# Optimization experiments

Hardware: AMD Instinct MI355X
Metric: run time of the kernel (lower is better)

The kernel has to match this reference:

```python
import jax, jax.numpy as jnp
import numpy as np

T, D, N = 131072, 512, 8


def setup_inputs() -> dict:
    key = jax.random.key(0)
    k1, k2, k3, k4 = jax.random.split(key, 4)
    x = jax.random.normal(k1, (T, D), dtype=jnp.float32)
    branch_idx = jax.random.randint(k2, (T,), 0, N, dtype=jnp.int32)
    # module inits weight to identity and bias to zero; use random values
    # (scaled like a trained projection) for a meaningful correctness test
    weight = jax.random.normal(k3, (N, D, D), dtype=jnp.float32) * (1.0 / np.sqrt(D))
    bias = jax.random.normal(k4, (N, D), dtype=jnp.float32) * 0.02
    return {"x": x, "branch_idx": branch_idx, "weight": weight, "bias": bias}


def reference(x, branch_idx, weight, bias):
    # Math: out[t] = x[t] @ weight[branch_idx[t]] + bias[branch_idx[t]]
    # Instead of materializing the gathered (T, D, D) weight tensor (as the
    # naive torch code does), run one dense GEMM per branch and select the
    # rows belonging to that branch. Same result, far less HBM traffic.
    num_branches = weight.shape[0]
    out = jnp.take(bias, branch_idx, axis=0)  # (T, D) gathered bias
    for n in range(num_branches):  # small fixed loop over branches
        mask = (branch_idx == n)[:, None]  # (T, 1)
        out = out + jnp.where(mask, x @ weight[n], jnp.zeros((), x.dtype))
    return out
```

## Files before the change

### kernel.cpp

```cpp
#include <hip/hip_runtime.h>
#include <hip/hip_bf16.h>
#include <stdint.h>

#define T_TOK 131072
#define DIM   512
#define NBR   8
#define BM    64
#define BK    32
#define NKT   (DIM / BK)
#define GT    512
#define MT    288

typedef __attribute__((ext_vector_type(8))) __bf16 bf16x8;
typedef __attribute__((ext_vector_type(4))) float  f32x4;
typedef unsigned short ushort_t;

__device__ __forceinline__ unsigned short f2bf(float f) {
  union { float f; unsigned int u; } v; v.f = f;
  unsigned int r = v.u + 0x7fffu + ((v.u >> 16) & 1u);
  return (unsigned short)(r >> 16);
}


__global__ void k_init(int* counts) {
  if (threadIdx.x < NBR) counts[threadIdx.x] = 0;
}

__global__ __launch_bounds__(512) void k_bhist(const int* __restrict__ bidx,
                                               int* __restrict__ counts) {
  __shared__ int h[NBR];
  if (threadIdx.x < NBR) h[threadIdx.x] = 0;
  __syncthreads();
  int t = blockIdx.x * 512 + threadIdx.x;
  atomicAdd(&h[bidx[t]], 1);
  __syncthreads();
  if (threadIdx.x < NBR) atomicAdd(&counts[threadIdx.x], h[threadIdx.x]);
}

__global__ void k_off(const int* __restrict__ counts, int* __restrict__ offsets,
                      int* __restrict__ cursors) {
  if (threadIdx.x == 0) {
    int s = 0;
    for (int n = 0; n < NBR; ++n) { offsets[n] = s; cursors[n] = s; s += counts[n]; }
  }
}

__global__ __launch_bounds__(512) void k_scatter(const int* __restrict__ bidx,
                                                 int* __restrict__ cursors,
                                                 int* __restrict__ perm) {
  __shared__ int h[NBR], base[NBR];
  if (threadIdx.x < NBR) h[threadIdx.x] = 0;
  __syncthreads();
  int t = blockIdx.x * 512 + threadIdx.x;
  int b = bidx[t];
  int rank = atomicAdd(&h[b], 1);
  __syncthreads();
  if (threadIdx.x < NBR)
    base[threadIdx.x] = atomicAdd(&cursors[threadIdx.x], h[threadIdx.x]);
  __syncthreads();
  perm[base[b] + rank] = t;
}

__global__ __launch_bounds__(256) void k_wtrans(const float* __restrict__ W,
                                                ushort_t* __restrict__ Wt) {
  __shared__ float tile[BK][129];
  int blk = blockIdx.x;
  int b  = blk >> 6;
  int kt = (blk >> 2) & 15;
  int cb = blk & 3;
  int t = threadIdx.x;
  #pragma unroll
  for (int i = 0; i < 4; ++i) {
    int idx4 = i * 256 + t;
    int kr = idx4 >> 5;
    int c4 = idx4 & 31;
    const float* src = W + (((size_t)b * DIM + (size_t)(kt * BK + kr)) * DIM + cb * 128 + c4 * 4);
    float4 v = *(const float4*)src;
    tile[kr][c4 * 4 + 0] = v.x;
    tile[kr][c4 * 4 + 1] = v.y;
    tile[kr][c4 * 4 + 2] = v.z;
    tile[kr][c4 * 4 + 3] = v.w;
  }
  __syncthreads();
  int c  = t >> 1;
  int kh = t & 1;
  unsigned int p[8];
  #pragma unroll
  for (int i = 0; i < 8; ++i) {
    unsigned short lo = f2bf(tile[kh * 16 + i * 2 + 0][c]);
    unsigned short hi = f2bf(tile[kh * 16 + i * 2 + 1][c]);
    p[i] = (unsigned int)lo | ((unsigned int)hi << 16);
  }
  size_t obase = (((size_t)b * 16 + kt) * DIM + (size_t)(cb * 128 + c)) * BK + kh * 16;
  uint4 q0; q0.x = p[0]; q0.y = p[1]; q0.z = p[2]; q0.w = p[3];
  uint4 q1; q1.x = p[4]; q1.y = p[5]; q1.z = p[6]; q1.w = p[7];
  *(uint4*)&Wt[obase]     = q0;
  *(uint4*)&Wt[obase + 8] = q1;
}

__global__ __launch_bounds__(GT, 4)
void k_gemm(const float* __restrict__ x, const float* __restrict__ bias,
            const ushort_t* __restrict__ Wt,
            const int* __restrict__ counts, const int* __restrict__ offsets,
            const int* __restrict__ perm, float* __restrict__ out) {
  __shared__ __align__(16) ushort_t As[NKT * 4 * 64 * 8];
  __shared__ int rowIdx[BM];

  const int tid = threadIdx.x;
  const int l = tid & 63;
  const int w = tid >> 6;

  const int b  = blockIdx.x / MT;
  const int lt = blockIdx.x % MT;
  const int cnt = counts[b];
  const int row0 = lt * BM;
  if (row0 >= cnt) return;
  const int gstart = offsets[b];
  const int vrows = min(BM, cnt - row0);

  if (tid < BM) {
    int r = row0 + tid; if (r >= cnt) r = cnt - 1;
    rowIdx[tid] = perm[gstart + r];
  }
  __syncthreads();

  const int arow = tid >> 3;
  const int kq = tid & 7;
  const float* aptr = x + (size_t)rowIdx[arow] * DIM + kq * 4;
  const int wbase = (((arow >> 4) * 64) + (kq >> 1) * 16 + (arow & 15)) * 8 + (kq & 1) * 4;

  {
    float4 xa = *(const float4*)aptr;
    float4 xb = *(const float4*)(aptr + BK);
    #pragma unroll
    for (int i = 0; i < NKT; ++i) {
      float4 xn;
      if (i + 2 < NKT) xn = *(const float4*)(aptr + (i + 2) * BK);
      ushort4 a4;
      a4.x = f2bf(xa.x); a4.y = f2bf(xa.y); a4.z = f2bf(xa.z); a4.w = f2bf(xa.w);
      *(ushort4*)&As[i * 2048 + wbase] = a4;
      xa = xb; xb = xn;
    }
  }
  __syncthreads();

  const ushort_t* wtile = Wt + (size_t)b * (NKT * BK * DIM);
  int bBase[4];
  #pragma unroll
  for (int cf = 0; cf < 4; ++cf)
    bBase[cf] = (w * 64 + cf * 16 + (l & 15)) * BK + (l >> 4) * 8;

  f32x4 acc[4][4];
  #pragma unroll
  for (int rf = 0; rf < 4; ++rf)
    #pragma unroll
    for (int cf = 0; cf < 4; ++cf) acc[rf][cf] = (f32x4){0.f, 0.f, 0.f, 0.f};

  bf16x8 bq[4];
  #pragma unroll
  for (int cf = 0; cf < 4; ++cf) bq[cf] = *(const bf16x8*)(wtile + bBase[cf]);

  #pragma unroll
  for (int kt = 0; kt < NKT; ++kt) {
    bf16x8 bqn[4];
    if (kt + 1 < NKT) {
      const ushort_t* wtk = wtile + (kt + 1) * (BK * DIM);
      #pragma unroll
      for (int cf = 0; cf < 4; ++cf) bqn[cf] = *(const bf16x8*)(wtk + bBase[cf]);
    }
    bf16x8 af[4];
    #pragma unroll
    for (int rf = 0; rf < 4; ++rf)
      af[rf] = *(const bf16x8*)&As[(kt * 4 + rf) * 512 + l * 8];
    #pragma unroll
    for (int cf = 0; cf < 4; ++cf)
      #pragma unroll
      for (int rf = 0; rf < 4; ++rf)
        acc[rf][cf] = __builtin_amdgcn_mfma_f32_16x16x32_bf16(af[rf], bq[cf], acc[rf][cf], 0, 0, 0);
    if (kt + 1 < NKT) {
      #pragma unroll
      for (int cf = 0; cf < 4; ++cf) bq[cf] = bqn[cf];
    }
  }

  float bv[4];
  #pragma unroll
  for (int cf = 0; cf < 4; ++cf) bv[cf] = bias[b * DIM + w * 64 + cf * 16 + (l & 15)];
  const int rb = (l >> 4) * 4;
  #pragma unroll
  for (int rf = 0; rf < 4; ++rf) {
    #pragma unroll
    for (int j = 0; j < 4; ++j) {
      int r = rf * 16 + rb + j;
      if (r < vrows) {
        float* op = out + (size_t)rowIdx[r] * DIM + w * 64 + (l & 15);
        #pragma unroll
        for (int cf = 0; cf < 4; ++cf) op[cf * 16] = acc[rf][cf][j] + bv[cf];
      }
    }
  }
}

extern "C" void kernel_launch(void* const* d_in, const int* in_sizes, int n_in,
                              void* d_out, int out_size, void* d_ws, size_t ws_size,
                              hipStream_t stream) {
  const float* x    = (const float*)d_in[0];
  const int*   bidx = (const int*)d_in[1];
  const float* W    = (const float*)d_in[2];
  const float* bias = (const float*)d_in[3];
  float* out = (float*)d_out;

  char* ws = (char*)d_ws;
  int* counts  = (int*)(ws + 0);
  int* cursors = (int*)(ws + 64);
  int* offsets = (int*)(ws + 128);
  int* perm    = (int*)(ws + 256);
  ushort_t* Wt = (ushort_t*)(ws + (1u << 20));

  k_init<<<1, 64, 0, stream>>>(counts);
  k_bhist<<<T_TOK / 512, 512, 0, stream>>>(bidx, counts);
  k_off<<<1, 64, 0, stream>>>(counts, offsets, cursors);
  k_scatter<<<T_TOK / 512, 512, 0, stream>>>(bidx, cursors, perm);
  k_wtrans<<<512, 256, 0, stream>>>(W, Wt);
  k_gemm<<<NBR * MT, GT, 0, stream>>>(x, bias, Wt, counts, offsets, perm, out);
}
```

Baseline: 205.8 us.

## Coalesce gathered x loads and stage output through swizzled LDS for float4 stores

```diff
diff --git a/kernel.cpp b/kernel.cpp
--- a/kernel.cpp
+++ b/kernel.cpp
@@ -105,6 +105,7 @@
             const int* __restrict__ perm, float* __restrict__ out) {
   __shared__ __align__(16) ushort_t As[NKT * 4 * 64 * 8];
   __shared__ int rowIdx[BM];
+  float* Ot = (float*)As;
 
   const int tid = threadIdx.x;
   const int l = tid & 63;
@@ -124,22 +125,31 @@
   }
   __syncthreads();
 
-  const int arow = tid >> 3;
-  const int kq = tid & 7;
-  const float* aptr = x + (size_t)rowIdx[arow] * DIM + kq * 4;
-  const int wbase = (((arow >> 4) * 64) + (kq >> 1) * 16 + (arow & 15)) * 8 + (kq & 1) * 4;
-
   {
-    float4 xa = *(const float4*)aptr;
-    float4 xb = *(const float4*)(aptr + BK);
-    #pragma unroll
-    for (int i = 0; i < NKT; ++i) {
-      float4 xn;
-      if (i + 2 < NKT) xn = *(const float4*)(aptr + (i + 2) * BK);
-      ushort4 a4;
-      a4.x = f2bf(xa.x); a4.y = f2bf(xa.y); a4.z = f2bf(xa.z); a4.w = f2bf(xa.w);
-      *(ushort4*)&As[i * 2048 + wbase] = a4;
-      xa = xb; xb = xn;
+    float4 v[8][2];
+    #pragma unroll
+    for (int j = 0; j < 8; ++j) {
+      const float* rp = x + (size_t)rowIdx[w * 8 + j] * DIM;
+      #pragma unroll
+      for (int i = 0; i < 2; ++i)
+        v[j][i] = *(const float4*)(rp + i * 256 + l * 4);
+    }
+    const int rf  = w >> 1;
+    const int Llo = (w & 1) * 8;
+    const int Lhi = (l & 7) >> 1;
+    const int e0  = (l & 1) * 4;
+    const int ktl = l >> 3;
+    #pragma unroll
+    for (int j = 0; j < 8; ++j) {
+      #pragma unroll
+      for (int i = 0; i < 2; ++i) {
+        int f = (i * 8 + ktl) * 4 + rf;
+        int slot = (Lhi * 16 + Llo + j) ^ ktl;
+        ushort4 a4;
+        a4.x = f2bf(v[j][i].x); a4.y = f2bf(v[j][i].y);
+        a4.z = f2bf(v[j][i].z); a4.w = f2bf(v[j][i].w);
+        *(ushort4*)&As[f * 512 + slot * 8 + e0] = a4;
+      }
     }
   }
   __syncthreads();
@@ -168,10 +178,11 @@
       #pragma unroll
       for (int cf = 0; cf < 4; ++cf) bqn[cf] = *(const bf16x8*)(wtk + bBase[cf]);
     }
+    const int lsw = (l ^ (kt & 7)) * 8;
     bf16x8 af[4];
     #pragma unroll
     for (int rf = 0; rf < 4; ++rf)
-      af[rf] = *(const bf16x8*)&As[(kt * 4 + rf) * 512 + l * 8];
+      af[rf] = *(const bf16x8*)&As[(kt * 4 + rf) * 512 + lsw];
     #pragma unroll
     for (int cf = 0; cf < 4; ++cf)
       #pragma unroll
@@ -186,18 +197,40 @@
   float bv[4];
   #pragma unroll
   for (int cf = 0; cf < 4; ++cf) bv[cf] = bias[b * DIM + w * 64 + cf * 16 + (l & 15)];
-  const int rb = (l >> 4) * 4;
-  #pragma unroll
-  for (int rf = 0; rf < 4; ++rf) {
-    #pragma unroll
-    for (int j = 0; j < 4; ++j) {
-      int r = rf * 16 + rb + j;
-      if (r < vrows) {
-        float* op = out + (size_t)rowIdx[r] * DIM + w * 64 + (l & 15);
+
+  __syncthreads();
+  #pragma unroll
+  for (int p = 0; p < 2; ++p) {
+    #pragma unroll
+    for (int rr = 0; rr < 2; ++rr) {
+      int rf = p * 2 + rr;
+      #pragma unroll
+      for (int j = 0; j < 4; ++j) {
+        int rip = rr * 16 + (l >> 4) * 4 + j;
+        int sxk = (rip & 7) << 2;
         #pragma unroll
-        for (int cf = 0; cf < 4; ++cf) op[cf * 16] = acc[rf][cf][j] + bv[cf];
+        for (int cf = 0; cf < 4; ++cf) {
+          int col = w * 64 + cf * 16 + (l & 15);
+          Ot[rip * 512 + (col ^ sxk)] = acc[rf][cf][j] + bv[cf];
+        }
       }
     }
+    __syncthreads();
+    #pragma unroll
+    for (int q = 0; q < 4; ++q) {
+      int rip = w * 4 + q;
+      int grow = p * 32 + rip;
+      if (grow < vrows) {
+        float* op = out + (size_t)rowIdx[grow] * DIM;
+        int s = rip & 7;
+        #pragma unroll
+        for (int h = 0; h < 2; ++h) {
+          float4 vv = *(const float4*)&Ot[rip * 512 + h * 256 + l * 4];
+          *(float4*)(op + h * 256 + ((l ^ s) * 4)) = vv;
+        }
+      }
+    }
+    if (p == 0) __syncthreads();
   }
 }
 
```

Result: slower. 220.9 us (+7.3%).

## Make grouped GEMM persistent with prefetched double-buffered A tiles

Applied to the files above, without the earlier changes.

```diff
diff --git a/kernel.cpp b/kernel.cpp
--- a/kernel.cpp
+++ b/kernel.cpp
@@ -5,11 +5,13 @@
 #define T_TOK 131072
 #define DIM   512
 #define NBR   8
-#define BM    64
+#define BM    32
 #define BK    32
 #define NKT   (DIM / BK)
 #define GT    512
-#define MT    288
+#define MTS   544
+#define NTILE (NBR * MTS)
+#define GRID  1024
 
 typedef __attribute__((ext_vector_type(8))) __bf16 bf16x8;
 typedef __attribute__((ext_vector_type(4))) float  f32x4;
@@ -103,101 +105,147 @@
             const ushort_t* __restrict__ Wt,
             const int* __restrict__ counts, const int* __restrict__ offsets,
             const int* __restrict__ perm, float* __restrict__ out) {
-  __shared__ __align__(16) ushort_t As[NKT * 4 * 64 * 8];
-  __shared__ int rowIdx[BM];
+  __shared__ __align__(16) ushort_t As[2][NKT * 2 * 512];
 
   const int tid = threadIdx.x;
   const int l = tid & 63;
   const int w = tid >> 6;
 
-  const int b  = blockIdx.x / MT;
-  const int lt = blockIdx.x % MT;
-  const int cnt = counts[b];
-  const int row0 = lt * BM;
-  if (row0 >= cnt) return;
-  const int gstart = offsets[b];
-  const int vrows = min(BM, cnt - row0);
-
-  if (tid < BM) {
-    int r = row0 + tid; if (r >= cnt) r = cnt - 1;
-    rowIdx[tid] = perm[gstart + r];
-  }
-  __syncthreads();
-
-  const int arow = tid >> 3;
-  const int kq = tid & 7;
-  const float* aptr = x + (size_t)rowIdx[arow] * DIM + kq * 4;
-  const int wbase = (((arow >> 4) * 64) + (kq >> 1) * 16 + (arow & 15)) * 8 + (kq & 1) * 4;
-
+  int cur_t = blockIdx.x;
+  for (;;) {
+    if (cur_t >= NTILE) return;
+    int b = cur_t / MTS, lt = cur_t - b * MTS;
+    if (lt * BM < counts[b]) break;
+    cur_t += GRID;
+  }
+
+  float4 v[4][2];
   {
-    float4 xa = *(const float4*)aptr;
-    float4 xb = *(const float4*)(aptr + BK);
-    #pragma unroll
-    for (int i = 0; i < NKT; ++i) {
-      float4 xn;
-      if (i + 2 < NKT) xn = *(const float4*)(aptr + (i + 2) * BK);
-      ushort4 a4;
-      a4.x = f2bf(xa.x); a4.y = f2bf(xa.y); a4.z = f2bf(xa.z); a4.w = f2bf(xa.w);
-      *(ushort4*)&As[i * 2048 + wbase] = a4;
-      xa = xb; xb = xn;
-    }
-  }
-  __syncthreads();
-
-  const ushort_t* wtile = Wt + (size_t)b * (NKT * BK * DIM);
-  int bBase[4];
-  #pragma unroll
-  for (int cf = 0; cf < 4; ++cf)
-    bBase[cf] = (w * 64 + cf * 16 + (l & 15)) * BK + (l >> 4) * 8;
-
-  f32x4 acc[4][4];
-  #pragma unroll
-  for (int rf = 0; rf < 4; ++rf)
-    #pragma unroll
-    for (int cf = 0; cf < 4; ++cf) acc[rf][cf] = (f32x4){0.f, 0.f, 0.f, 0.f};
-
-  bf16x8 bq[4];
-  #pragma unroll
-  for (int cf = 0; cf < 4; ++cf) bq[cf] = *(const bf16x8*)(wtile + bBase[cf]);
-
-  #pragma unroll
-  for (int kt = 0; kt < NKT; ++kt) {
-    bf16x8 bqn[4];
-    if (kt + 1 < NKT) {
-      const ushort_t* wtk = wtile + (kt + 1) * (BK * DIM);
-      #pragma unroll
-      for (int cf = 0; cf < 4; ++cf) bqn[cf] = *(const bf16x8*)(wtk + bBase[cf]);
-    }
-    bf16x8 af[4];
-    #pragma unroll
-    for (int rf = 0; rf < 4; ++rf)
-      af[rf] = *(const bf16x8*)&As[(kt * 4 + rf) * 512 + l * 8];
+    int b = cur_t / MTS, lt = cur_t - b * MTS;
+    int cnt = counts[b], g0 = offsets[b];
+    #pragma unroll
+    for (int j = 0; j < 4; ++j) {
+      int r = lt * BM + w * 4 + j;
+      int rr = perm[g0 + (r < cnt ? r : cnt - 1)];
+      const float* rp = x + (size_t)rr * DIM;
+      v[j][0] = *(const float4*)(rp + l * 4);
+      v[j][1] = *(const float4*)(rp + 256 + l * 4);
+    }
+  }
+
+  int cur = 0;
+  for (;;) {
+    int next_t = cur_t + GRID;
+    for (;;) {
+      if (next_t >= NTILE) break;
+      int b = next_t / MTS, lt = next_t - b * MTS;
+      if (lt * BM < counts[b]) break;
+      next_t += GRID;
+    }
+
+    {
+      const int q  = (l & 7) >> 1;
+      const int e0 = (l & 1) * 4;
+      const int h  = l >> 3;
+      const int rf = w >> 2;
+      #pragma unroll
+      for (int j = 0; j < 4; ++j) {
+        const int rlow = (w * 4 + j) & 15;
+        #pragma unroll
+        for (int i = 0; i < 2; ++i) {
+          int kt = i * 8 + h;
+          int Ls = (q * 16 + rlow) ^ h;
+          ushort4 a4;
+          a4.x = f2bf(v[j][i].x); a4.y = f2bf(v[j][i].y);
+          a4.z = f2bf(v[j][i].z); a4.w = f2bf(v[j][i].w);
+          *(ushort4*)&As[cur][(kt * 2 + rf) * 512 + Ls * 8 + e0] = a4;
+        }
+      }
+    }
+    __syncthreads();
+
+    if (next_t < NTILE) {
+      int b = next_t / MTS, lt = next_t - b * MTS;
+      int cnt = counts[b], g0 = offsets[b];
+      #pragma unroll
+      for (int j = 0; j < 4; ++j) {
+        int r = lt * BM + w * 4 + j;
+        int rr = perm[g0 + (r < cnt ? r : cnt - 1)];
+        const float* rp = x + (size_t)rr * DIM;
+        v[j][0] = *(const float4*)(rp + l * 4);
+        v[j][1] = *(const float4*)(rp + 256 + l * 4);
+      }
+    }
+
+    const int bcur = cur_t / MTS;
+    const ushort_t* wtile = Wt + (size_t)bcur * (NKT * BK * DIM);
+    int bBase[4];
     #pragma unroll
     for (int cf = 0; cf < 4; ++cf)
-      #pragma unroll
-      for (int rf = 0; rf < 4; ++rf)
-        acc[rf][cf] = __builtin_amdgcn_mfma_f32_16x16x32_bf16(af[rf], bq[cf], acc[rf][cf], 0, 0, 0);
-    if (kt + 1 < NKT) {
-      #pragma unroll
-      for (int cf = 0; cf < 4; ++cf) bq[cf] = bqn[cf];
-    }
-  }
-
-  float bv[4];
-  #pragma unroll
-  for (int cf = 0; cf < 4; ++cf) bv[cf] = bias[b * DIM + w * 64 + cf * 16 + (l & 15)];
-  const int rb = (l >> 4) * 4;
-  #pragma unroll
-  for (int rf = 0; rf < 4; ++rf) {
-    #pragma unroll
-    for (int j = 0; j < 4; ++j) {
-      int r = rf * 16 + rb + j;
-      if (r < vrows) {
-        float* op = out + (size_t)rowIdx[r] * DIM + w * 64 + (l & 15);
-        #pragma unroll
-        for (int cf = 0; cf < 4; ++cf) op[cf * 16] = acc[rf][cf][j] + bv[cf];
-      }
-    }
+      bBase[cf] = (w * 64 + cf * 16 + (l & 15)) * BK + (l >> 4) * 8;
+
+    f32x4 acc[2][4];
+    #pragma unroll
+    for (int rf = 0; rf < 2; ++rf)
+      #pragma unroll
+      for (int cf = 0; cf < 4; ++cf) acc[rf][cf] = (f32x4){0.f, 0.f, 0.f, 0.f};
+
+    bf16x8 bq[4];
+    #pragma unroll
+    for (int cf = 0; cf < 4; ++cf) bq[cf] = *(const bf16x8*)(wtile + bBase[cf]);
+
+    const ushort_t* asrc = &As[cur][0];
+    #pragma unroll
+    for (int kt = 0; kt < NKT; ++kt) {
+      bf16x8 bqn[4];
+      if (kt + 1 < NKT) {
+        const ushort_t* wtk = wtile + (kt + 1) * (BK * DIM);
+        #pragma unroll
+        for (int cf = 0; cf < 4; ++cf) bqn[cf] = *(const bf16x8*)(wtk + bBase[cf]);
+      }
+      const int lsw = (l ^ (kt & 7)) * 8;
+      bf16x8 af[2];
+      #pragma unroll
+      for (int rf = 0; rf < 2; ++rf)
+        af[rf] = *(const bf16x8*)&asrc[(kt * 2 + rf) * 512 + lsw];
+      #pragma unroll
+      for (int cf = 0; cf < 4; ++cf)
+        #pragma unroll
+        for (int rf = 0; rf < 2; ++rf)
+          acc[rf][cf] = __builtin_amdgcn_mfma_f32_16x16x32_bf16(af[rf], bq[cf], acc[rf][cf], 0, 0, 0);
+      if (kt + 1 < NKT) {
+        #pragma unroll
+        for (int cf = 0; cf < 4; ++cf) bq[cf] = bqn[cf];
+      }
+    }
+
+    {
+      const int ltc = cur_t - bcur * MTS;
+      const int cnt = counts[bcur];
+      const int vrows = min(BM, cnt - ltc * BM);
+      const int g0 = offsets[bcur] + ltc * BM;
+      float bv[4];
+      #pragma unroll
+      for (int cf = 0; cf < 4; ++cf)
+        bv[cf] = bias[bcur * DIM + w * 64 + cf * 16 + (l & 15)];
+      #pragma unroll
+      for (int rf = 0; rf < 2; ++rf) {
+        #pragma unroll
+        for (int j = 0; j < 4; ++j) {
+          int r = rf * 16 + (l >> 4) * 4 + j;
+          if (r < vrows) {
+            int orow = perm[g0 + r];
+            float* op = out + (size_t)orow * DIM + w * 64 + (l & 15);
+            #pragma unroll
+            for (int cf = 0; cf < 4; ++cf) op[cf * 16] = acc[rf][cf][j] + bv[cf];
+          }
+        }
+      }
+    }
+
+    if (next_t >= NTILE) return;
+    cur_t = next_t;
+    cur ^= 1;
   }
 }
 
@@ -222,5 +270,5 @@
   k_off<<<1, 64, 0, stream>>>(counts, offsets, cursors);
   k_scatter<<<T_TOK / 512, 512, 0, stream>>>(bidx, cursors, perm);
   k_wtrans<<<512, 256, 0, stream>>>(W, Wt);
-  k_gemm<<<NBR * MT, GT, 0, stream>>>(x, bias, Wt, counts, offsets, perm, out);
-}
+  k_gemm<<<GRID, GT, 0, stream>>>(x, bias, Wt, counts, offsets, perm, out);
+}
```

New measurement: 266.7 us. +29.6%, slower.

## Replace global branch sort with per-window local sort and pre-converted bf16 x

Applied to the files above, without the earlier changes.

```diff
diff --git a/kernel.cpp b/kernel.cpp
--- a/kernel.cpp
+++ b/kernel.cpp
@@ -5,11 +5,12 @@
 #define T_TOK 131072
 #define DIM   512
 #define NBR   8
-#define BM    64
+#define WIN   512
+#define NWIN  (T_TOK / WIN)
+#define SLCAP 640
+#define NSL   40
 #define BK    32
 #define NKT   (DIM / BK)
-#define GT    512
-#define MT    288
 
 typedef __attribute__((ext_vector_type(8))) __bf16 bf16x8;
 typedef __attribute__((ext_vector_type(4))) float  f32x4;
@@ -19,46 +20,6 @@
   union { float f; unsigned int u; } v; v.f = f;
   unsigned int r = v.u + 0x7fffu + ((v.u >> 16) & 1u);
   return (unsigned short)(r >> 16);
-}
-
-
-__global__ void k_init(int* counts) {
-  if (threadIdx.x < NBR) counts[threadIdx.x] = 0;
-}
-
-__global__ __launch_bounds__(512) void k_bhist(const int* __restrict__ bidx,
-                                               int* __restrict__ counts) {
-  __shared__ int h[NBR];
-  if (threadIdx.x < NBR) h[threadIdx.x] = 0;
-  __syncthreads();
-  int t = blockIdx.x * 512 + threadIdx.x;
-  atomicAdd(&h[bidx[t]], 1);
-  __syncthreads();
-  if (threadIdx.x < NBR) atomicAdd(&counts[threadIdx.x], h[threadIdx.x]);
-}
-
-__global__ void k_off(const int* __restrict__ counts, int* __restrict__ offsets,
-                      int* __restrict__ cursors) {
-  if (threadIdx.x == 0) {
-    int s = 0;
-    for (int n = 0; n < NBR; ++n) { offsets[n] = s; cursors[n] = s; s += counts[n]; }
-  }
-}
-
-__global__ __launch_bounds__(512) void k_scatter(const int* __restrict__ bidx,
-                                                 int* __restrict__ cursors,
-                                                 int* __restrict__ perm) {
-  __shared__ int h[NBR], base[NBR];
-  if (threadIdx.x < NBR) h[threadIdx.x] = 0;
-  __syncthreads();
-  int t = blockIdx.x * 512 + threadIdx.x;
-  int b = bidx[t];
-  int rank = atomicAdd(&h[b], 1);
-  __syncthreads();
-  if (threadIdx.x < NBR)
-    base[threadIdx.x] = atomicAdd(&cursors[threadIdx.x], h[threadIdx.x]);
-  __syncthreads();
-  perm[base[b] + rank] = t;
 }
 
 __global__ __launch_bounds__(256) void k_wtrans(const float* __restrict__ W,
@@ -98,104 +59,160 @@
   *(uint4*)&Wt[obase + 8] = q1;
 }
 
-__global__ __launch_bounds__(GT, 4)
-void k_gemm(const float* __restrict__ x, const float* __restrict__ bias,
-            const ushort_t* __restrict__ Wt,
-            const int* __restrict__ counts, const int* __restrict__ offsets,
-            const int* __restrict__ perm, float* __restrict__ out) {
-  __shared__ __align__(16) ushort_t As[NKT * 4 * 64 * 8];
-  __shared__ int rowIdx[BM];
-
-  const int tid = threadIdx.x;
-  const int l = tid & 63;
-  const int w = tid >> 6;
-
-  const int b  = blockIdx.x / MT;
-  const int lt = blockIdx.x % MT;
-  const int cnt = counts[b];
-  const int row0 = lt * BM;
-  if (row0 >= cnt) return;
-  const int gstart = offsets[b];
-  const int vrows = min(BM, cnt - row0);
-
-  if (tid < BM) {
-    int r = row0 + tid; if (r >= cnt) r = cnt - 1;
-    rowIdx[tid] = perm[gstart + r];
-  }
-  __syncthreads();
-
-  const int arow = tid >> 3;
-  const int kq = tid & 7;
-  const float* aptr = x + (size_t)rowIdx[arow] * DIM + kq * 4;
-  const int wbase = (((arow >> 4) * 64) + (kq >> 1) * 16 + (arow & 15)) * 8 + (kq & 1) * 4;
-
-  {
-    float4 xa = *(const float4*)aptr;
-    float4 xb = *(const float4*)(aptr + BK);
-    #pragma unroll
-    for (int i = 0; i < NKT; ++i) {
-      float4 xn;
-      if (i + 2 < NKT) xn = *(const float4*)(aptr + (i + 2) * BK);
-      ushort4 a4;
-      a4.x = f2bf(xa.x); a4.y = f2bf(xa.y); a4.z = f2bf(xa.z); a4.w = f2bf(xa.w);
-      *(ushort4*)&As[i * 2048 + wbase] = a4;
-      xa = xb; xb = xn;
-    }
-  }
-  __syncthreads();
-
-  const ushort_t* wtile = Wt + (size_t)b * (NKT * BK * DIM);
-  int bBase[4];
+__global__ __launch_bounds__(WIN) void k_sort(const int* __restrict__ bidx,
+                                              unsigned short* __restrict__ smap,
+                                              int* __restrict__ sliceBr,
+                                              int* __restrict__ tsArr) {
+  __shared__ int cnt[NBR], ps[NBR], rankL[WIN], bidL[WIN];
+  const int w = blockIdx.x;
+  const int t = threadIdx.x;
+  if (t < NBR) cnt[t] = 0;
+  __syncthreads();
+  int b = bidx[w * WIN + t];
+  bidL[t] = b;
+  rankL[t] = atomicAdd(&cnt[b], 1);
+  __syncthreads();
+  if (t == 0) {
+    int s = 0;
+    for (int g = 0; g < NBR; ++g) { ps[g] = s; s += (cnt[g] + 15) >> 4; }
+    tsArr[w] = s;
+  }
+  __syncthreads();
+  if (t < NSL) {
+    int br = -1;
+    #pragma unroll
+    for (int g = 0; g < NBR; ++g) {
+      int sc = (cnt[g] + 15) >> 4;
+      if (t >= ps[g] && t < ps[g] + sc) br = g;
+    }
+    sliceBr[w * NSL + t] = br;
+  }
+  smap[w * WIN + t] = (unsigned short)(ps[bidL[t]] * 16 + rankL[t]);
+}
+
+__global__ __launch_bounds__(512) void k_xcvt(const float* __restrict__ x,
+                                              const unsigned short* __restrict__ smap,
+                                              ushort_t* __restrict__ xT, int w0) {
+  __shared__ unsigned short slotL[WIN];
+  const int bid = blockIdx.x;
+  const int w = w0 + (bid >> 2);
+  const int part = bid & 3;
+  const int t = threadIdx.x;
+  slotL[t] = smap[w * WIN + t];
+  __syncthreads();
+  const float4* xp = (const float4*)(x + (size_t)w * (WIN * DIM));
+  ushort_t* xTw = xT + (size_t)(w - w0) * (NKT * SLCAP * BK);
+  #pragma unroll 4
+  for (int i = 0; i < 32; ++i) {
+    int fidx = part * 16384 + i * 512 + t;
+    float4 v = xp[fidx];
+    int row = fidx >> 7;
+    int kq4 = fidx & 127;
+    int kt = kq4 >> 3;
+    int kk = (kq4 & 7) * 4;
+    int slot = slotL[row];
+    ushort4 a4;
+    a4.x = f2bf(v.x); a4.y = f2bf(v.y); a4.z = f2bf(v.z); a4.w = f2bf(v.w);
+    *(ushort4*)&xTw[((size_t)kt * SLCAP + slot) * BK + kk] = a4;
+  }
+}
+
+__global__ __launch_bounds__(1024, 4)
+void k_gemm(const ushort_t* __restrict__ xT, const ushort_t* __restrict__ Wt,
+            const float* __restrict__ bias,
+            const unsigned short* __restrict__ smap,
+            const int* __restrict__ sliceBr, const int* __restrict__ tsArr,
+            float* __restrict__ out, int w0, int WCcur) {
+  __shared__ float OtL[128 * 130];
+  __shared__ int sbrL[NSL];
+
+  const int bid = blockIdx.x;
+  const int wloc = bid % WCcur;
+  const int cb = bid / WCcur;
+  const int w = w0 + wloc;
+  const int t = threadIdx.x;
+  const int l = t & 63;
+  const int wv = t >> 6;
+  const int ts = tsArr[w];
+
+  if (t < NSL) sbrL[t] = sliceBr[w * NSL + t];
+  const unsigned short myslot = smap[w * WIN + (t & 511)];
+  __syncthreads();
+
+  const int sg = wv >> 1;
+  const int ch = wv & 1;
+  const int colbase = cb * 128 + ch * 64;
+
+  const ushort_t* xTw = xT + (size_t)wloc * (NKT * SLCAP * BK);
+  const int aoff = (l & 15) * BK + (l >> 4) * 8;
+  int boff[4];
   #pragma unroll
   for (int cf = 0; cf < 4; ++cf)
-    bBase[cf] = (w * 64 + cf * 16 + (l & 15)) * BK + (l >> 4) * 8;
-
-  f32x4 acc[4][4];
-  #pragma unroll
-  for (int rf = 0; rf < 4; ++rf)
-    #pragma unroll
-    for (int cf = 0; cf < 4; ++cf) acc[rf][cf] = (f32x4){0.f, 0.f, 0.f, 0.f};
-
-  bf16x8 bq[4];
-  #pragma unroll
-  for (int cf = 0; cf < 4; ++cf) bq[cf] = *(const bf16x8*)(wtile + bBase[cf]);
-
-  #pragma unroll
+    boff[cf] = (colbase + cf * 16 + (l & 15)) * BK + (l >> 4) * 8;
+
+  f32x4 acc[5][4];
+  #pragma unroll
+  for (int s = 0; s < 5; ++s)
+    #pragma unroll
+    for (int cf = 0; cf < 4; ++cf) acc[s][cf] = (f32x4){0.f, 0.f, 0.f, 0.f};
+
   for (int kt = 0; kt < NKT; ++kt) {
-    bf16x8 bqn[4];
-    if (kt + 1 < NKT) {
-      const ushort_t* wtk = wtile + (kt + 1) * (BK * DIM);
+    const ushort_t* aplane = xTw + (size_t)kt * (SLCAP * BK);
+    int curbr = -1;
+    bf16x8 bq[4];
+    #pragma unroll
+    for (int s = 0; s < 5; ++s) {
+      const int gs = sg * 5 + s;
+      if (gs < ts) {
+        int br = sbrL[gs];
+        if (br != curbr) {
+          curbr = br;
+          const ushort_t* wp = Wt + ((size_t)br * NKT + kt) * (DIM * BK);
+          #pragma unroll
+          for (int cf = 0; cf < 4; ++cf) bq[cf] = *(const bf16x8*)(wp + boff[cf]);
+        }
+        bf16x8 af = *(const bf16x8*)(aplane + gs * 512 + aoff);
+        #pragma unroll
+        for (int cf = 0; cf < 4; ++cf)
+          acc[s][cf] = __builtin_amdgcn_mfma_f32_16x16x32_bf16(af, bq[cf], acc[s][cf], 0, 0, 0);
+      }
+    }
+  }
+
+  const int row = t & 511;
+  const int half = t >> 9;
+  float* op = out + ((size_t)w * WIN + row) * DIM + cb * 128 + half * 64;
+
+  #pragma unroll
+  for (int p = 0; p < 5; ++p) {
+    __syncthreads();
+    #pragma unroll
+    for (int s = 0; s < 5; ++s) {
+      const int gs = sg * 5 + s;
+      if (gs >= 8 * p && gs < 8 * p + 8 && gs < ts) {
+        const int br = sbrL[gs];
+        float bv[4];
+        #pragma unroll
+        for (int cf = 0; cf < 4; ++cf)
+          bv[cf] = bias[br * DIM + colbase + cf * 16 + (l & 15)];
+        const int lr0 = (gs - 8 * p) * 16 + (l >> 4) * 4;
+        #pragma unroll
+        for (int j = 0; j < 4; ++j)
+          #pragma unroll
+          for (int cf = 0; cf < 4; ++cf)
+            OtL[(lr0 + j) * 130 + ch * 64 + cf * 16 + (l & 15)] = acc[s][cf][j] + bv[cf];
+      }
+    }
+    __syncthreads();
+    const int lp = (int)myslot - p * 128;
+    if (lp >= 0 && lp < 128) {
+      const float* lsrc = &OtL[lp * 130 + half * 64];
       #pragma unroll
-      for (int cf = 0; cf < 4; ++cf) bqn[cf] = *(const bf16x8*)(wtk + bBase[cf]);
-    }
-    bf16x8 af[4];
-    #pragma unroll
-    for (int rf = 0; rf < 4; ++rf)
-      af[rf] = *(const bf16x8*)&As[(kt * 4 + rf) * 512 + l * 8];
-    #pragma unroll
-    for (int cf = 0; cf < 4; ++cf)
-      #pragma unroll
-      for (int rf = 0; rf < 4; ++rf)
-        acc[rf][cf] = __builtin_amdgcn_mfma_f32_16x16x32_bf16(af[rf], bq[cf], acc[rf][cf], 0, 0, 0);
-    if (kt + 1 < NKT) {
-      #pragma unroll
-      for (int cf = 0; cf < 4; ++cf) bq[cf] = bqn[cf];
-    }
-  }
-
-  float bv[4];
-  #pragma unroll
-  for (int cf = 0; cf < 4; ++cf) bv[cf] = bias[b * DIM + w * 64 + cf * 16 + (l & 15)];
-  const int rb = (l >> 4) * 4;
-  #pragma unroll
-  for (int rf = 0; rf < 4; ++rf) {
-    #pragma unroll
-    for (int j = 0; j < 4; ++j) {
-      int r = rf * 16 + rb + j;
-      if (r < vrows) {
-        float* op = out + (size_t)rowIdx[r] * DIM + w * 64 + (l & 15);
-        #pragma unroll
-        for (int cf = 0; cf < 4; ++cf) op[cf * 16] = acc[rf][cf][j] + bv[cf];
+      for (int q = 0; q < 16; ++q) {
+        float2 e0 = *(const float2*)(lsrc + q * 4);
+        float2 e1 = *(const float2*)(lsrc + q * 4 + 2);
+        float4 vv; vv.x = e0.x; vv.y = e0.y; vv.z = e1.x; vv.w = e1.y;
+        *(float4*)(op + q * 4) = vv;
       }
     }
   }
@@ -211,16 +228,24 @@
   float* out = (float*)d_out;
 
   char* ws = (char*)d_ws;
-  int* counts  = (int*)(ws + 0);
-  int* cursors = (int*)(ws + 64);
-  int* offsets = (int*)(ws + 128);
-  int* perm    = (int*)(ws + 256);
-  ushort_t* Wt = (ushort_t*)(ws + (1u << 20));
-
-  k_init<<<1, 64, 0, stream>>>(counts);
-  k_bhist<<<T_TOK / 512, 512, 0, stream>>>(bidx, counts);
-  k_off<<<1, 64, 0, stream>>>(counts, offsets, cursors);
-  k_scatter<<<T_TOK / 512, 512, 0, stream>>>(bidx, cursors, perm);
+  ushort_t* Wt = (ushort_t*)ws;
+  unsigned short* smap = (unsigned short*)(ws + (4u << 20));
+  int* sliceBr = (int*)(ws + (4u << 20) + 262144);
+  int* tsArr   = (int*)(ws + (4u << 20) + 262144 + 40960);
+  ushort_t* xT = (ushort_t*)(ws + (5u << 20));
+
+  const size_t perWin = (size_t)NKT * SLCAP * BK * 2;
+  size_t avail = ws_size > (5u << 20) ? ws_size - (5u << 20) : 0;
+  int WC = 8;
+  const int opts[6] = {256, 128, 64, 32, 16, 8};
+  for (int i = 0; i < 6; ++i) {
+    if ((size_t)opts[i] * perWin <= avail) { WC = opts[i]; break; }
+  }
+
   k_wtrans<<<512, 256, 0, stream>>>(W, Wt);
-  k_gemm<<<NBR * MT, GT, 0, stream>>>(x, bias, Wt, counts, offsets, perm, out);
-}
+  k_sort<<<NWIN, WIN, 0, stream>>>(bidx, smap, sliceBr, tsArr);
+  for (int w0 = 0; w0 < NWIN; w0 += WC) {
+    k_xcvt<<<WC * 4, 512, 0, stream>>>(x, smap, xT, w0);
+    k_gemm<<<WC * 4, 1024, 0, stream>>>(xT, Wt, bias, smap, sliceBr, tsArr, out, w0, WC);
+  }
+}
```

Measured after the change: 385.9 us. +87.5%, slower.
